# Kernel tuning notes

Measured on AMD Instinct MI355X. Metric: run time of the kernel, lower is better.

The kernel has to match this reference:

```python
import jax, jax.numpy as jnp
import numpy as np

N_NODES, N_EDGES, NUM_GRAPHS = 50000, 800000, 64
F_DIM, H_DIM, N_LAYERS, N_CLASSES = 64, 64, 3, 16
EPS = 1e-5  # StdAggregation epsilon (PyG)


def setup_inputs() -> dict:
    key = jax.random.key(0)
    ks = jax.random.split(key, 12)
    s = 0.05
    x = jax.random.normal(ks[0], (N_NODES, F_DIM), jnp.float32)
    edge_index = jax.random.randint(ks[1], (2, N_EDGES), 0, N_NODES, dtype=jnp.int32)
    batch = jnp.sort(jax.random.randint(ks[2], (N_NODES,), 0, NUM_GRAPHS, dtype=jnp.int32))
    # per-layer PNAConv params (towers=1): pre Linear(2F->F), post Linear(13F->H), lin Linear(H->H)
    pre_w = jax.random.normal(ks[3], (N_LAYERS, F_DIM, 2 * F_DIM), jnp.float32) * s
    pre_b = jnp.zeros((N_LAYERS, F_DIM), jnp.float32)
    post_w = jax.random.normal(ks[4], (N_LAYERS, H_DIM, 13 * F_DIM), jnp.float32) * s
    post_b = jnp.zeros((N_LAYERS, H_DIM), jnp.float32)
    lin_w = jax.random.normal(ks[5], (N_LAYERS, H_DIM, H_DIM), jnp.float32) * s
    lin_b = jnp.zeros((N_LAYERS, H_DIM), jnp.float32)
    mlp_w1 = jax.random.normal(ks[6], (H_DIM, H_DIM), jnp.float32) * s
    mlp_b1 = jnp.zeros((H_DIM,), jnp.float32)
    mlp_w2 = jax.random.normal(ks[7], (N_CLASSES, H_DIM), jnp.float32) * s
    mlp_b2 = jnp.zeros((N_CLASSES,), jnp.float32)
    return dict(x=x, edge_index=edge_index, batch=batch,
                pre_w=pre_w, pre_b=pre_b, post_w=post_w, post_b=post_b,
                lin_w=lin_w, lin_b=lin_b, mlp_w1=mlp_w1, mlp_b1=mlp_b1,
                mlp_w2=mlp_w2, mlp_b2=mlp_b2)


def pna_forward(x, src, dst, pre_w, pre_b, post_w, post_b, lin_w, lin_b,
                mlp_w1, mlp_b1, mlp_w2, mlp_b2, batch):
    N = x.shape[0]
    deg_raw = jax.ops.segment_sum(jnp.ones_like(src, jnp.float32), dst, N)  # in-degree [N]
    deg = jnp.maximum(deg_raw, 1.0)[:, None]
    # avg log degree (PNA avg_deg['log'] from the degree histogram of this graph)
    avg_log = jnp.mean(jnp.log(deg_raw + 1.0))
    log_deg = jnp.log(deg + 1.0)
    amp = log_deg / avg_log          # amplification scaler [N,1]
    att = avg_log / log_deg          # attenuation scaler [N,1]
    has_in = (deg_raw > 0)[:, None]

    for l in range(pre_w.shape[0]):
        h = jnp.concatenate([x[dst], x[src]], axis=-1)        # [E, 2F] (x_i, x_j)
        m = h @ pre_w[l].T + pre_b[l]                          # pre_nn message [E, F]
        s1 = jax.ops.segment_sum(m, dst, N)
        s2 = jax.ops.segment_sum(m * m, dst, N)
        mean = s1 / deg
        std = jnp.sqrt(jax.nn.relu(s2 / deg - mean * mean) + EPS)
        mn = jnp.where(has_in, jax.ops.segment_min(m, dst, N), 0.0)
        mx = jnp.where(has_in, jax.ops.segment_max(m, dst, N), 0.0)
        aggr = jnp.concatenate([mean, mn, mx, std], axis=-1)   # [N, 4F]
        out = jnp.concatenate([x, aggr, aggr * amp, aggr * att], axis=-1)  # [N, 13F]
        out = out @ post_w[l].T + post_b[l]                    # post_nn [N, H]
        x = jax.nn.relu(out @ lin_w[l].T + lin_b[l])           # conv.lin + outer ReLU

    # global mean pool over graphs
    counts = jnp.maximum(
        jax.ops.segment_sum(jnp.ones((N,), x.dtype), batch, NUM_GRAPHS), 1.0)
    g = jax.ops.segment_sum(x, batch, NUM_GRAPHS) / counts[:, None]  # [G, H]
    g = jax.nn.relu(g @ mlp_w1.T + mlp_b1)
    return g @ mlp_w2.T + mlp_b2                               # [G, C]


def reference(x, edge_index, batch, pre_w, pre_b, post_w, post_b,
              lin_w, lin_b, mlp_w1, mlp_b1, mlp_w2, mlp_b2):
    src, dst = edge_index[0], edge_index[1]
    return pna_forward(x, src, dst, pre_w, pre_b, post_w, post_b,
                       lin_w, lin_b, mlp_w1, mlp_b1, mlp_w2, mlp_b2, batch)
```

## Files before the change

### kernel.cpp

```cpp
#include <hip/hip_runtime.h>
#include <math.h>

#define N_NODES   50000
#define N_EDGES   800000
#define NUM_GRAPHS 64
#define FDIM      64
#define HDIM      64
#define NLAYERS   3
#define NCLASSES  16
#define EPS       1e-5f

#define SCAN_CHUNK 1024
#define NCHUNKS ((N_NODES + SCAN_CHUNK - 1) / SCAN_CHUNK)

typedef unsigned short u16;
typedef unsigned int   u32;
typedef __attribute__((ext_vector_type(8))) short short8;
typedef __attribute__((ext_vector_type(4))) float floatx4;

#define WKS_LAYER 159744
#define PRES_LAYER 24576

__device__ inline void split1(float f, u16& h, u16& m, u16& l) {
    u32 b  = __float_as_uint(f);
    u32 hb = b & 0xFFFF0000u;
    float r = f - __uint_as_float(hb);
    u32 mb = __float_as_uint(r) & 0xFFFF0000u;
    float r2 = r - __uint_as_float(mb);
    u32 lb = __float_as_uint(r2) & 0xFFFF0000u;
    h = (u16)(hb >> 16); m = (u16)(mb >> 16); l = (u16)(lb >> 16);
}

__device__ inline void gl_lds16(const void* g, void* l) {
    __builtin_amdgcn_global_load_lds(
        (const __attribute__((address_space(1))) u32*)g,
        (__attribute__((address_space(3))) u32*)l, 16, 0, 0);
}

__global__ __launch_bounds__(256) void k_comb(const float* __restrict__ post_w,
                                              const float* __restrict__ lin_w,
                                              const float* __restrict__ pre_w,
                                              const float* __restrict__ post_b,
                                              const float* __restrict__ lin_b,
                                              u16* __restrict__ WkS,
                                              u16* __restrict__ PreS,
                                              float* __restrict__ bcv,
                                              int* __restrict__ cnt,
                                              float* __restrict__ logsum) {
    int b = blockIdx.x, t = threadIdx.x;
    int zi = b * 256 + t;
    if (zi < N_NODES) cnt[zi] = 0;
    if (zi == 0) *logsum = 0.f;

    if (b < 624) {
        int c  = t & 63;
        int kl = t >> 6;
        int l  = b / 208;
        int o  = (b % 208) * 4 + kl;
        const float* lw = lin_w + (size_t)l * 4096 + c * 64;
        const float* pw = post_w + (size_t)l * 53248 + o;
        float acc = 0.f;
        #pragma unroll 8
        for (int j = 0; j < 64; ++j)
            acc += lw[j] * pw[(size_t)j * 832];
        u16 h, m, lo;
        split1(acc, h, m, lo);

        int kn;
        if (o < 64) kn = o;
        else {
            int s  = (o - 64) >> 8;
            int mm = (o - 64) & 255;
            int j  = mm >> 5, r = mm & 31;
            kn = 64 + j * 96 + s * 32 + r;
        }
        int ch  = kn >> 5;
        int kin = kn & 31;
        int n16 = c & 15, nt = c >> 4;
        int swk = (((kin >> 3) + (n16 >> 1)) & 3) * 8 + (kin & 7);
        size_t base = (size_t)l * WKS_LAYER + (size_t)ch * 6144
                    + nt * 512 + n16 * 32 + swk;
        WkS[base]        = h;
        WkS[base + 2048] = m;
        WkS[base + 4096] = lo;
    } else if (b == 624) {
        if (t < 192) {
            int l = t >> 6, c = t & 63;
            float acc = lin_b[l * 64 + c];
            for (int j = 0; j < 64; ++j)
                acc += lin_w[(size_t)l * 4096 + c * 64 + j] * post_b[l * 64 + j];
            bcv[l * 64 + c] = acc;
        }
    } else {
        int i = (b - 625) * 256 + t;
        int l = i >> 13;
        int rem = i & 8191;
        int c128 = rem >> 6;
        int k = rem & 63;
        float v;
        if (c128 < 64) v = pre_w[(size_t)l * 8192 + c128 * 128 + k];
        else           v = pre_w[(size_t)l * 8192 + (c128 - 64) * 128 + 64 + k];
        u16 h, m, lo;
        split1(v, h, m, lo);
        int ch = k >> 5, kin = k & 31;
        int nt = c128 >> 4, n16 = c128 & 15;
        int swk = (((kin >> 3) + (n16 >> 1)) & 3) * 8 + (kin & 7);
        size_t base = (size_t)l * PRES_LAYER + (size_t)ch * 12288
                    + nt * 512 + n16 * 32 + swk;
        PreS[base]        = h;
        PreS[base + 4096] = m;
        PreS[base + 8192] = lo;
    }
}

__global__ void k_count(const int* __restrict__ dst, int* __restrict__ cnt,
                        int* __restrict__ rank) {
    int e = blockIdx.x * 256 + threadIdx.x;
    if (e < N_EDGES) rank[e] = atomicAdd(&cnt[dst[e]], 1);
}

__global__ void k_chunk_sums(const int* __restrict__ cnt, int* __restrict__ bsum,
                             float* __restrict__ logsum) {
    __shared__ int   ired[256];
    __shared__ float lred[256];
    int b = blockIdx.x, t = threadIdx.x;
    int base = b * SCAN_CHUNK;
    int s = 0; float ls = 0.f;
    for (int i = t; i < SCAN_CHUNK; i += 256) {
        int idx = base + i;
        if (idx < N_NODES) {
            int v = cnt[idx];
            s += v;
            ls += logf((float)v + 1.0f);
        }
    }
    ired[t] = s; lred[t] = ls;
    __syncthreads();
    for (int off = 128; off > 0; off >>= 1) {
        if (t < off) { ired[t] += ired[t + off]; lred[t] += lred[t + off]; }
        __syncthreads();
    }
    if (t == 0) { bsum[b] = ired[0]; atomicAdd(logsum, lred[0]); }
}

__global__ void k_scan_top(const int* __restrict__ bsum, int* __restrict__ boff,
                           int* __restrict__ row_start) {
    if (threadIdx.x == 0) {
        int acc = 0;
        for (int i = 0; i < NCHUNKS; ++i) { boff[i] = acc; acc += bsum[i]; }
        row_start[N_NODES] = acc;
    }
}

__global__ void k_scan_chunks(const int* __restrict__ cnt, const int* __restrict__ boff,
                              int* __restrict__ row_start) {
    __shared__ int tsum[256];
    int b = blockIdx.x, t = threadIdx.x;
    int base = b * SCAN_CHUNK + t * 4;
    int v[4]; int s = 0;
    #pragma unroll
    for (int i = 0; i < 4; ++i) {
        int idx = base + i;
        v[i] = (idx < N_NODES) ? cnt[idx] : 0;
        s += v[i];
    }
    tsum[t] = s;
    __syncthreads();
    for (int off = 1; off < 256; off <<= 1) {
        int val = (t >= off) ? tsum[t - off] : 0;
        __syncthreads();
        tsum[t] += val;
        __syncthreads();
    }
    int excl = boff[b] + tsum[t] - s;
    #pragma unroll
    for (int i = 0; i < 4; ++i) {
        int idx = base + i;
        if (idx < N_NODES) row_start[idx] = excl;
        excl += v[i];
    }
}

__global__ void k_scatter(const int* __restrict__ src, const int* __restrict__ dst,
                          const int* __restrict__ rank,
                          const int* __restrict__ row_start,
                          int* __restrict__ csr_src) {
    int e = blockIdx.x * 256 + threadIdx.x;
    if (e < N_EDGES) {
        int d = dst[e];
        csr_src[row_start[d] + rank[e]] = src[e];
    }
}

__global__ void k_scal(const int* __restrict__ cnt, const float* __restrict__ logsum,
                       float* __restrict__ inv_deg, float* __restrict__ ampv,
                       float* __restrict__ attv, float* __restrict__ g_sum,
                       int* __restrict__ g_cnt) {
    int n = blockIdx.x * 256 + threadIdx.x;
    if (blockIdx.x == 0) {
        for (int i = threadIdx.x; i < 4096; i += 256) g_sum[i] = 0.f;
        if (threadIdx.x < 64) g_cnt[threadIdx.x] = 0;
    }
    if (n < N_NODES) {
        float avg = logsum[0] / (float)N_NODES;
        float degf = fmaxf((float)cnt[n], 1.0f);
        inv_deg[n] = 1.0f / degf;
        float ld = logf(degf + 1.0f);
        ampv[n] = ld / avg;
        attv[n] = avg / ld;
    }
}

__global__ __launch_bounds__(256, 4) void k_pre(const float* __restrict__ x,
                                                const u16* __restrict__ PreS,
                                                const float* __restrict__ pre_b,
                                                float* __restrict__ p,
                                                float* __restrict__ q) {
    __shared__ u16 ldsB[2 * 12288];
    int t = threadIdx.x;
    int w = t >> 6;
    int lane = t & 63;
    int m = lane & 15;
    int qh = lane >> 4;
    int rowBase = blockIdx.x * 64;

    int myrow = rowBase + 16 * w + m;
    bool vr = myrow < N_NODES;
    int crow = vr ? myrow : 0;
    const float* xrow = x + (size_t)crow * 64;

    int bo = m * 32 + ((qh + (m >> 1)) & 3) * 8;

    #pragma unroll
    for (int ch = 0; ch < 2; ++ch) {
        const char* g = (const char*)PreS + (size_t)ch * 24576 + w * 6144 + lane * 16;
        char* l = (char*)ldsB + ch * 24576 + w * 6144;
        #pragma unroll
        for (int i = 0; i < 6; ++i)
            gl_lds16(g + i * 1024, l + i * 1024);
    }
    float fa[2][8];
    #pragma unroll
    for (int ch = 0; ch < 2; ++ch) {
        const float* sp = xrow + ch * 32 + qh * 8;
        float4 u0 = *(const float4*)sp;
        float4 u1 = *(const float4*)(sp + 4);
        fa[ch][0] = vr ? u0.x : 0.f; fa[ch][1] = vr ? u0.y : 0.f;
        fa[ch][2] = vr ? u0.z : 0.f; fa[ch][3] = vr ? u0.w : 0.f;
        fa[ch][4] = vr ? u1.x : 0.f; fa[ch][5] = vr ? u1.y : 0.f;
        fa[ch][6] = vr ? u1.z : 0.f; fa[ch][7] = vr ? u1.w : 0.f;
    }
    asm volatile("s_waitcnt vmcnt(0)" ::: "memory");
    __syncthreads();

    floatx4 acc[8] = {};
    #pragma unroll
    for (int ch = 0; ch < 2; ++ch) {
        union { u32 u[4]; short8 s8; } AH, AM, AL;
        #pragma unroll
        for (int i = 0; i < 4; ++i) {
            float f0 = fa[ch][2 * i], f1 = fa[ch][2 * i + 1];
            u32 b0 = __float_as_uint(f0), b1 = __float_as_uint(f1);
            u32 h0 = b0 & 0xFFFF0000u,  h1 = b1 & 0xFFFF0000u;
            float r0 = f0 - __uint_as_float(h0);
            float r1 = f1 - __uint_as_float(h1);
            u32 m0 = __float_as_uint(r0) & 0xFFFF0000u;
            u32 m1 = __float_as_uint(r1) & 0xFFFF0000u;
            float s0 = r0 - __uint_as_float(m0);
            float s1 = r1 - __uint_as_float(m1);
            u32 l0 = __float_as_uint(s0) & 0xFFFF0000u;
            u32 l1 = __float_as_uint(s1) & 0xFFFF0000u;
            AH.u[i] = (h0 >> 16) | h1;
            AM.u[i] = (m0 >> 16) | m1;
            AL.u[i] = (l0 >> 16) | l1;
        }
        const u16* Bb = ldsB + ch * 12288;
        #pragma unroll
        for (int nt = 0; nt < 8; ++nt) {
            short8 bH = *(const short8*)(Bb + nt * 512 + bo);
            short8 bM = *(const short8*)(Bb + 4096 + nt * 512 + bo);
            short8 bL = *(const short8*)(Bb + 8192 + nt * 512 + bo);
            acc[nt] = __builtin_amdgcn_mfma_f32_16x16x32_bf16(AH.s8, bH, acc[nt], 0, 0, 0);
            acc[nt] = __builtin_amdgcn_mfma_f32_16x16x32_bf16(AH.s8, bM, acc[nt], 0, 0, 0);
            acc[nt] = __builtin_amdgcn_mfma_f32_16x16x32_bf16(AM.s8, bH, acc[nt], 0, 0, 0);
            acc[nt] = __builtin_amdgcn_mfma_f32_16x16x32_bf16(AH.s8, bL, acc[nt], 0, 0, 0);
            acc[nt] = __builtin_amdgcn_mfma_f32_16x16x32_bf16(AM.s8, bM, acc[nt], 0, 0, 0);
            acc[nt] = __builtin_amdgcn_mfma_f32_16x16x32_bf16(AL.s8, bH, acc[nt], 0, 0, 0);
        }
    }

    int col = m;
    #pragma unroll
    for (int nt = 0; nt < 8; ++nt) {
        int cbase = (nt & 3) * 16 + col;
        float bias = (nt < 4) ? pre_b[cbase] : 0.f;
        float* outp = (nt < 4) ? p : q;
        #pragma unroll
        for (int reg = 0; reg < 4; ++reg) {
            int grow = rowBase + 16 * w + qh * 4 + reg;
            if (grow < N_NODES)
                outp[(size_t)grow * 64 + cbase] = acc[nt][reg] + bias;
        }
    }
}

__global__ __launch_bounds__(256) void k_aggr(const float* __restrict__ p,
                                              const float* __restrict__ q,
                                              const int* __restrict__ row_start,
                                              const int* __restrict__ csr_src,
                                              const float* __restrict__ inv_deg,
                                              float* __restrict__ aggr) {
    int wid  = (blockIdx.x * 256 + threadIdx.x) >> 6;
    int lane = threadIdx.x & 63;
    if (wid >= N_NODES) return;
    int n = wid;
    int beg = row_start[n], end = row_start[n + 1];
    float sum = 0.f, sq = 0.f;
    float mn = INFINITY, mx = -INFINITY;
    int e = beg;
    for (; e + 7 < end; e += 8) {
        float qv[8];
        #pragma unroll
        for (int u = 0; u < 8; ++u) {
            int s = csr_src[e + u];
            qv[u] = q[(size_t)s * 64 + lane];
        }
        #pragma unroll
        for (int u = 0; u < 8; ++u) {
            float m = qv[u];
            sum += m; sq += m * m;
            mn = fminf(mn, m); mx = fmaxf(mx, m);
        }
    }
    for (; e + 3 < end; e += 4) {
        float qv[4];
        #pragma unroll
        for (int u = 0; u < 4; ++u) {
            int s = csr_src[e + u];
            qv[u] = q[(size_t)s * 64 + lane];
        }
        #pragma unroll
        for (int u = 0; u < 4; ++u) {
            float m = qv[u];
            sum += m; sq += m * m;
            mn = fminf(mn, m); mx = fmaxf(mx, m);
        }
    }
    for (; e < end; ++e) {
        int s = csr_src[e];
        float m = q[(size_t)s * 64 + lane];
        sum += m; sq += m * m;
        mn = fminf(mn, m); mx = fmaxf(mx, m);
    }
    float* a = aggr + (size_t)n * 256;
    if (end <= beg) {
        a[lane]       = 0.f;
        a[64 + lane]  = 0.f;
        a[128 + lane] = 0.f;
        a[192 + lane] = sqrtf(EPS);
    } else {
        float pv = p[n * 64 + lane];
        float id = inv_deg[n];
        float meanq = sum * id;
        float var = fmaxf(sq * id - meanq * meanq, 0.f);
        a[lane]       = pv + meanq;
        a[64 + lane]  = pv + mn;
        a[128 + lane] = pv + mx;
        a[192 + lane] = sqrtf(var + EPS);
    }
}

#define DOMFMA(ACC0, ACC1)                                                     \
    {                                                                          \
        _Pragma("unroll")                                                      \
        for (int nt = 0; nt < 4; ++nt) {                                       \
            short8 bH = *(const short8*)(Bb + nt * 512 + bo);                  \
            short8 bM = *(const short8*)(Bb + 2048 + nt * 512 + bo);           \
            short8 bL = *(const short8*)(Bb + 4096 + nt * 512 + bo);           \
            ACC0[nt] = __builtin_amdgcn_mfma_f32_16x16x32_bf16(AH0.s8, bH, ACC0[nt], 0, 0, 0); \
            ACC0[nt] = __builtin_amdgcn_mfma_f32_16x16x32_bf16(AH0.s8, bM, ACC0[nt], 0, 0, 0); \
            ACC0[nt] = __builtin_amdgcn_mfma_f32_16x16x32_bf16(AM0.s8, bH, ACC0[nt], 0, 0, 0); \
            ACC0[nt] = __builtin_amdgcn_mfma_f32_16x16x32_bf16(AH0.s8, bL, ACC0[nt], 0, 0, 0); \
            ACC0[nt] = __builtin_amdgcn_mfma_f32_16x16x32_bf16(AM0.s8, bM, ACC0[nt], 0, 0, 0); \
            ACC0[nt] = __builtin_amdgcn_mfma_f32_16x16x32_bf16(AL0.s8, bH, ACC0[nt], 0, 0, 0); \
            ACC1[nt] = __builtin_amdgcn_mfma_f32_16x16x32_bf16(AH1.s8, bH, ACC1[nt], 0, 0, 0); \
            ACC1[nt] = __builtin_amdgcn_mfma_f32_16x16x32_bf16(AH1.s8, bM, ACC1[nt], 0, 0, 0); \
            ACC1[nt] = __builtin_amdgcn_mfma_f32_16x16x32_bf16(AM1.s8, bH, ACC1[nt], 0, 0, 0); \
            ACC1[nt] = __builtin_amdgcn_mfma_f32_16x16x32_bf16(AH1.s8, bL, ACC1[nt], 0, 0, 0); \
            ACC1[nt] = __builtin_amdgcn_mfma_f32_16x16x32_bf16(AM1.s8, bM, ACC1[nt], 0, 0, 0); \
            ACC1[nt] = __builtin_amdgcn_mfma_f32_16x16x32_bf16(AL1.s8, bH, ACC1[nt], 0, 0, 0); \
        }                                                                      \
    }

__global__ __launch_bounds__(256, 2) void k_post(const float* __restrict__ x,
                                                 const float* __restrict__ aggr,
                                                 const float* __restrict__ ampv,
                                                 const float* __restrict__ attv,
                                                 const u16* __restrict__ WkS,
                                                 const float* __restrict__ bc,
                                                 float* __restrict__ xout) {
    __shared__ u16 ldsB[3 * 6144];
    int t = threadIdx.x;
    int w = t >> 6;
    int lane = t & 63;
    int m = lane & 15;
    int qh = lane >> 4;
    int rowBase = blockIdx.x * 128;

    int row0 = rowBase + 32 * w + m;
    int row1 = row0 + 16;
    int cr0 = (row0 < N_NODES) ? row0 : 0;
    int cr1 = (row1 < N_NODES) ? row1 : 0;
    const float* xr0 = x + (size_t)cr0 * 64;
    const float* xr1 = x + (size_t)cr1 * 64;
    const float* ar0 = aggr + (size_t)cr0 * 256;
    const float* ar1 = aggr + (size_t)cr1 * 256;

    int bo = m * 32 + ((qh + (m >> 1)) & 3) * 8;

    floatx4 accP0[4] = {}, accA0[4] = {}, accT0[4] = {};
    floatx4 accP1[4] = {}, accA1[4] = {}, accT1[4] = {};

    float f0[8], f1[8];
    union U8 { u32 u[4]; short8 s8; };
    U8 AH0, AM0, AL0, AH1, AM1, AL1;

    auto gptr = [&](int g, const float* xr, const float* ar) -> const float* {
        return (g < 2) ? (xr + 32 * g) : (ar + (g - 2) * 32);
    };
    auto loadRaw = [&](const float* sp, float* f) {
        float4 u0 = *(const float4*)(sp + qh * 8);
        float4 u1 = *(const float4*)(sp + qh * 8 + 4);
        f[0] = u0.x; f[1] = u0.y; f[2] = u0.z; f[3] = u0.w;
        f[4] = u1.x; f[5] = u1.y; f[6] = u1.z; f[7] = u1.w;
    };
    auto stageIssue = [&](int ch, int buf) {
        const char* g = (const char*)WkS + (size_t)ch * 12288 + w * 3072 + lane * 16;
        char* l = (char*)ldsB + buf * 12288 + w * 3072;
        #pragma unroll
        for (int i = 0; i < 3; ++i)
            gl_lds16(g + i * 1024, l + i * 1024);
    };
    auto split2 = [&](const float* f, U8& H, U8& M8, U8& L) {
        #pragma unroll
        for (int i = 0; i < 4; ++i) {
            float v0 = f[2 * i], v1 = f[2 * i + 1];
            u32 b0 = __float_as_uint(v0), b1 = __float_as_uint(v1);
            u32 h0 = b0 & 0xFFFF0000u,  h1 = b1 & 0xFFFF0000u;
            float r0 = v0 - __uint_as_float(h0);
            float r1 = v1 - __uint_as_float(h1);
            u32 m0 = __float_as_uint(r0) & 0xFFFF0000u;
            u32 m1 = __float_as_uint(r1) & 0xFFFF0000u;
            float s0 = r0 - __uint_as_float(m0);
            float s1 = r1 - __uint_as_float(m1);
            u32 l0 = __float_as_uint(s0) & 0xFFFF0000u;
            u32 l1 = __float_as_uint(s1) & 0xFFFF0000u;
            H.u[i]  = (h0 >> 16) | h1;
            M8.u[i] = (m0 >> 16) | m1;
            L.u[i]  = (l0 >> 16) | l1;
        }
    };

    loadRaw(gptr(0, xr0, ar0), f0);
    loadRaw(gptr(0, xr1, ar1), f1);
    stageIssue(0, 0);
    stageIssue(1, 1);
    asm volatile("s_waitcnt vmcnt(3)" ::: "memory");
    asm volatile("s_barrier" ::: "memory");

    for (int ch = 0; ch < 26; ++ch) {
        int s = (ch < 2) ? 0 : (ch - 2) % 3;
        if (s == 0) {
            split2(f0, AH0, AM0, AL0);
            split2(f1, AH1, AM1, AL1);
        }
        bool pf = (ch + 1 < 26) && ((ch + 1 < 2) || ((ch + 1 - 2) % 3 == 0));
        if (pf) {
            int gn = (ch + 1 < 2) ? (ch + 1) : (2 + (ch + 1 - 2) / 3);
            loadRaw(gptr(gn, xr0, ar0), f0);
            loadRaw(gptr(gn, xr1, ar1), f1);
        }
        int ch2 = (ch + 2 < 26) ? ch + 2 : ch + 2 - 26;
        stageIssue(ch2, (ch + 2) % 3);

        const u16* Bb = ldsB + (ch % 3) * 6144;
        if (s == 0)      { DOMFMA(accP0, accP1); }
        else if (s == 1) { DOMFMA(accA0, accA1); }
        else             { DOMFMA(accT0, accT1); }

        if (pf) asm volatile("s_waitcnt vmcnt(7)" ::: "memory");
        else    asm volatile("s_waitcnt vmcnt(3)" ::: "memory");
        asm volatile("s_barrier" ::: "memory");
    }

    int col = m;
    #pragma unroll
    for (int frag = 0; frag < 2; ++frag) {
        #pragma unroll
        for (int reg = 0; reg < 4; ++reg) {
            int grow = rowBase + 32 * w + 16 * frag + qh * 4 + reg;
            if (grow < N_NODES) {
                float av = ampv[grow], tv = attv[grow];
                #pragma unroll
                for (int nt = 0; nt < 4; ++nt) {
                    float pv = frag ? accP1[nt][reg] : accP0[nt][reg];
                    float av2 = frag ? accA1[nt][reg] : accA0[nt][reg];
                    float tv2 = frag ? accT1[nt][reg] : accT0[nt][reg];
                    float v = pv + av * av2 + tv * tv2 + bc[nt * 16 + col];
                    xout[(size_t)grow * 64 + nt * 16 + col] = fmaxf(v, 0.f);
                }
            }
        }
    }
}
#undef DOMFMA

__global__ __launch_bounds__(256) void k_pool(const float* __restrict__ x,
                                              const int* __restrict__ batch,
                                              float* __restrict__ g_sum,
                                              int* __restrict__ g_cnt) {
    int lane = threadIdx.x & 63;
    int wave = blockIdx.x * 4 + (threadIdx.x >> 6);
    const int NPW = 16;
    int beg = wave * NPW;
    if (beg >= N_NODES) return;
    int end = min(beg + NPW, N_NODES);
    float acc = 0.f;
    int cur = batch[beg];
    int c = 0;
    for (int n = beg; n < end; ++n) {
        int b = batch[n];
        if (b != cur) {
            atomicAdd(&g_sum[cur * 64 + lane], acc);
            if (lane == 0) atomicAdd(&g_cnt[cur], c);
            acc = 0.f; c = 0; cur = b;
        }
        acc += x[n * 64 + lane];
        ++c;
    }
    atomicAdd(&g_sum[cur * 64 + lane], acc);
    if (lane == 0) atomicAdd(&g_cnt[cur], c);
}

__global__ __launch_bounds__(256) void k_mlp(const float* __restrict__ g_sum,
                                             const int* __restrict__ g_cnt,
                                             const float* __restrict__ w1,
                                             const float* __restrict__ b1,
                                             const float* __restrict__ w2,
                                             const float* __restrict__ b2,
                                             float* __restrict__ out) {
    __shared__ float g[64][64];
    __shared__ float h[64][64];
    __shared__ float wT[64][65];
    int t = threadIdx.x;
    for (int idx = t; idx < 4096; idx += 256) {
        int gi = idx >> 6, c = idx & 63;
        float cntf = fmaxf((float)g_cnt[gi], 1.f);
        g[gi][c] = g_sum[idx] / cntf;
    }
    for (int idx = t; idx < 4096; idx += 256) {
        int c = idx >> 6, k = idx & 63;
        wT[k][c] = w1[c * 64 + k];
    }
    __syncthreads();
    for (int idx = t; idx < 4096; idx += 256) {
        int gi = idx >> 6, c = idx & 63;
        float acc = b1[c];
        for (int k = 0; k < 64; ++k) acc += g[gi][k] * wT[k][c];
        h[gi][c] = fmaxf(acc, 0.f);
    }
    __syncthreads();
    for (int idx = t; idx < 64 * NCLASSES; idx += 256) {
        int gi = idx >> 4, c = idx & 15;
        float acc = b2[c];
        for (int k = 0; k < 64; ++k) acc += h[gi][k] * w2[c * 64 + k];
        out[gi * NCLASSES + c] = acc;
    }
}

extern "C" void kernel_launch(void* const* d_in, const int* in_sizes, int n_in,
                              void* d_out, int out_size, void* d_ws, size_t ws_size,
                              hipStream_t stream) {
    const float* x      = (const float*)d_in[0];
    const int*   ei     = (const int*)d_in[1];
    const int*   batch  = (const int*)d_in[2];
    const float* pre_w  = (const float*)d_in[3];
    const float* pre_b  = (const float*)d_in[4];
    const float* post_w = (const float*)d_in[5];
    const float* post_b = (const float*)d_in[6];
    const float* lin_w  = (const float*)d_in[7];
    const float* lin_b  = (const float*)d_in[8];
    const float* mlp_w1 = (const float*)d_in[9];
    const float* mlp_b1 = (const float*)d_in[10];
    const float* mlp_w2 = (const float*)d_in[11];
    const float* mlp_b2 = (const float*)d_in[12];

    const int* src = ei;
    const int* dst = ei + N_EDGES;

    char* base = (char*)d_ws;
    size_t off = 0;
    auto alloc = [&](size_t bytes) -> void* {
        void* ptr = base + off;
        off += (bytes + 255) & ~(size_t)255;
        return ptr;
    };
    int*   cnt       = (int*)alloc(N_NODES * 4);
    int*   row_start = (int*)alloc((N_NODES + 1) * 4);
    int*   rank      = (int*)alloc(N_EDGES * 4);
    int*   csr_src   = (int*)alloc(N_EDGES * 4);
    int*   bsum      = (int*)alloc(64 * 4);
    int*   boff      = (int*)alloc(64 * 4);
    float* logsum    = (float*)alloc(16);
    float* inv_deg   = (float*)alloc(N_NODES * 4);
    float* ampv      = (float*)alloc(N_NODES * 4);
    float* attv      = (float*)alloc(N_NODES * 4);
    float* p         = (float*)alloc((size_t)N_NODES * 64 * 4);
    float* q         = (float*)alloc((size_t)N_NODES * 64 * 4);
    float* aggr      = (float*)alloc((size_t)N_NODES * 256 * 4);
    float* xb0       = (float*)alloc((size_t)N_NODES * 64 * 4);
    float* xb1       = (float*)alloc((size_t)N_NODES * 64 * 4);
    float* g_sum     = (float*)alloc(64 * 64 * 4);
    int*   g_cnt     = (int*)alloc(64 * 4);
    u16*   WkS       = (u16*)alloc((size_t)3 * WKS_LAYER * 2);
    u16*   PreS      = (u16*)alloc((size_t)3 * PRES_LAYER * 2);
    float* bcv       = (float*)alloc(3 * 64 * 4);

    k_comb<<<721, 256, 0, stream>>>(post_w, lin_w, pre_w, post_b, lin_b,
                                    WkS, PreS, bcv, cnt, logsum);

    k_count<<<(N_EDGES + 255) / 256, 256, 0, stream>>>(dst, cnt, rank);
    k_chunk_sums<<<NCHUNKS, 256, 0, stream>>>(cnt, bsum, logsum);
    k_scan_top<<<1, 64, 0, stream>>>(bsum, boff, row_start);
    k_scan_chunks<<<NCHUNKS, 256, 0, stream>>>(cnt, boff, row_start);
    k_scatter<<<(N_EDGES + 255) / 256, 256, 0, stream>>>(src, dst, rank,
                                                         row_start, csr_src);
    k_scal<<<(N_NODES + 255) / 256, 256, 0, stream>>>(cnt, logsum, inv_deg,
                                                      ampv, attv, g_sum, g_cnt);

    const int PRE_BLOCKS  = (N_NODES + 63) / 64;
    const int POST_BLOCKS = (N_NODES + 127) / 128;
    const float* xin = x;
    float* bufs[3] = {xb0, xb1, xb0};
    for (int l = 0; l < NLAYERS; ++l) {
        k_pre<<<PRE_BLOCKS, 256, 0, stream>>>(xin, PreS + (size_t)l * PRES_LAYER,
                                              pre_b + l * 64, p, q);
        k_aggr<<<(N_NODES + 3) / 4, 256, 0, stream>>>(p, q, row_start, csr_src,
                                                      inv_deg, aggr);
        float* xo = bufs[l];
        k_post<<<POST_BLOCKS, 256, 0, stream>>>(xin, aggr, ampv, attv,
                                                WkS + (size_t)l * WKS_LAYER,
                                                bcv + l * 64, xo);
        xin = xo;
    }

    int pool_waves = (N_NODES + 15) / 16;
    k_pool<<<(pool_waves + 3) / 4, 256, 0, stream>>>(xin, batch, g_sum, g_cnt);
    k_mlp<<<1, 256, 0, stream>>>(g_sum, g_cnt, mlp_w1, mlp_b1, mlp_w2, mlp_b2,
                                 (float*)d_out);
}
```

Before: 482.3 us.

## Read post weights directly from global memory in single-wave k_post blocks

k_post drops its triple-buffered LDS staging of the split bf16 weight chunks, along with the async global-to-LDS copies and per-chunk barriers. Each 64-thread single-wave block now handles 32 rows and loads its B fragments straight from global/L2 into registers before issuing the MFMAs. This removes barrier and LDS overhead and allows many more independent blocks. In exchange, every wave refetches the full weight set from cache with no cross-wave reuse, and the weight loads are no longer pipelined ahead of the compute.

Result: slower. 492.9 us (+2.2%).

```diff
diff --git a/kernel.cpp b/kernel.cpp
--- a/kernel.cpp
+++ b/kernel.cpp
@@ -370,44 +370,19 @@
     }
 }
 
-#define DOMFMA(ACC0, ACC1)                                                     \
-    {                                                                          \
-        _Pragma("unroll")                                                      \
-        for (int nt = 0; nt < 4; ++nt) {                                       \
-            short8 bH = *(const short8*)(Bb + nt * 512 + bo);                  \
-            short8 bM = *(const short8*)(Bb + 2048 + nt * 512 + bo);           \
-            short8 bL = *(const short8*)(Bb + 4096 + nt * 512 + bo);           \
-            ACC0[nt] = __builtin_amdgcn_mfma_f32_16x16x32_bf16(AH0.s8, bH, ACC0[nt], 0, 0, 0); \
-            ACC0[nt] = __builtin_amdgcn_mfma_f32_16x16x32_bf16(AH0.s8, bM, ACC0[nt], 0, 0, 0); \
-            ACC0[nt] = __builtin_amdgcn_mfma_f32_16x16x32_bf16(AM0.s8, bH, ACC0[nt], 0, 0, 0); \
-            ACC0[nt] = __builtin_amdgcn_mfma_f32_16x16x32_bf16(AH0.s8, bL, ACC0[nt], 0, 0, 0); \
-            ACC0[nt] = __builtin_amdgcn_mfma_f32_16x16x32_bf16(AM0.s8, bM, ACC0[nt], 0, 0, 0); \
-            ACC0[nt] = __builtin_amdgcn_mfma_f32_16x16x32_bf16(AL0.s8, bH, ACC0[nt], 0, 0, 0); \
-            ACC1[nt] = __builtin_amdgcn_mfma_f32_16x16x32_bf16(AH1.s8, bH, ACC1[nt], 0, 0, 0); \
-            ACC1[nt] = __builtin_amdgcn_mfma_f32_16x16x32_bf16(AH1.s8, bM, ACC1[nt], 0, 0, 0); \
-            ACC1[nt] = __builtin_amdgcn_mfma_f32_16x16x32_bf16(AM1.s8, bH, ACC1[nt], 0, 0, 0); \
-            ACC1[nt] = __builtin_amdgcn_mfma_f32_16x16x32_bf16(AH1.s8, bL, ACC1[nt], 0, 0, 0); \
-            ACC1[nt] = __builtin_amdgcn_mfma_f32_16x16x32_bf16(AM1.s8, bM, ACC1[nt], 0, 0, 0); \
-            ACC1[nt] = __builtin_amdgcn_mfma_f32_16x16x32_bf16(AL1.s8, bH, ACC1[nt], 0, 0, 0); \
-        }                                                                      \
-    }
-
-__global__ __launch_bounds__(256, 2) void k_post(const float* __restrict__ x,
-                                                 const float* __restrict__ aggr,
-                                                 const float* __restrict__ ampv,
-                                                 const float* __restrict__ attv,
-                                                 const u16* __restrict__ WkS,
-                                                 const float* __restrict__ bc,
-                                                 float* __restrict__ xout) {
-    __shared__ u16 ldsB[3 * 6144];
-    int t = threadIdx.x;
-    int w = t >> 6;
-    int lane = t & 63;
+__global__ __launch_bounds__(64) void k_post(const float* __restrict__ x,
+                                             const float* __restrict__ aggr,
+                                             const float* __restrict__ ampv,
+                                             const float* __restrict__ attv,
+                                             const u16* __restrict__ WkS,
+                                             const float* __restrict__ bc,
+                                             float* __restrict__ xout) {
+    int lane = threadIdx.x;
     int m = lane & 15;
     int qh = lane >> 4;
-    int rowBase = blockIdx.x * 128;
-
-    int row0 = rowBase + 32 * w + m;
+    int rowBase = blockIdx.x * 32;
+
+    int row0 = rowBase + m;
     int row1 = row0 + 16;
     int cr0 = (row0 < N_NODES) ? row0 : 0;
     int cr1 = (row1 < N_NODES) ? row1 : 0;
@@ -417,6 +392,7 @@
     const float* ar1 = aggr + (size_t)cr1 * 256;
 
     int bo = m * 32 + ((qh + (m >> 1)) & 3) * 8;
+    const u16* Wb = WkS + bo;
 
     floatx4 accP0[4] = {}, accA0[4] = {}, accT0[4] = {};
     floatx4 accP1[4] = {}, accA1[4] = {}, accT1[4] = {};
@@ -425,21 +401,11 @@
     union U8 { u32 u[4]; short8 s8; };
     U8 AH0, AM0, AL0, AH1, AM1, AL1;
 
-    auto gptr = [&](int g, const float* xr, const float* ar) -> const float* {
-        return (g < 2) ? (xr + 32 * g) : (ar + (g - 2) * 32);
-    };
     auto loadRaw = [&](const float* sp, float* f) {
         float4 u0 = *(const float4*)(sp + qh * 8);
         float4 u1 = *(const float4*)(sp + qh * 8 + 4);
         f[0] = u0.x; f[1] = u0.y; f[2] = u0.z; f[3] = u0.w;
         f[4] = u1.x; f[5] = u1.y; f[6] = u1.z; f[7] = u1.w;
-    };
-    auto stageIssue = [&](int ch, int buf) {
-        const char* g = (const char*)WkS + (size_t)ch * 12288 + w * 3072 + lane * 16;
-        char* l = (char*)ldsB + buf * 12288 + w * 3072;
-        #pragma unroll
-        for (int i = 0; i < 3; ++i)
-            gl_lds16(g + i * 1024, l + i * 1024);
     };
     auto split2 = [&](const float* f, U8& H, U8& M8, U8& L) {
         #pragma unroll
@@ -460,37 +426,46 @@
             L.u[i]  = (l0 >> 16) | l1;
         }
     };
-
-    loadRaw(gptr(0, xr0, ar0), f0);
-    loadRaw(gptr(0, xr1, ar1), f1);
-    stageIssue(0, 0);
-    stageIssue(1, 1);
-    asm volatile("s_waitcnt vmcnt(3)" ::: "memory");
-    asm volatile("s_barrier" ::: "memory");
-
-    for (int ch = 0; ch < 26; ++ch) {
-        int s = (ch < 2) ? 0 : (ch - 2) % 3;
-        if (s == 0) {
-            split2(f0, AH0, AM0, AL0);
-            split2(f1, AH1, AM1, AL1);
-        }
-        bool pf = (ch + 1 < 26) && ((ch + 1 < 2) || ((ch + 1 - 2) % 3 == 0));
-        if (pf) {
-            int gn = (ch + 1 < 2) ? (ch + 1) : (2 + (ch + 1 - 2) / 3);
-            loadRaw(gptr(gn, xr0, ar0), f0);
-            loadRaw(gptr(gn, xr1, ar1), f1);
-        }
-        int ch2 = (ch + 2 < 26) ? ch + 2 : ch + 2 - 26;
-        stageIssue(ch2, (ch + 2) % 3);
-
-        const u16* Bb = ldsB + (ch % 3) * 6144;
-        if (s == 0)      { DOMFMA(accP0, accP1); }
-        else if (s == 1) { DOMFMA(accA0, accA1); }
-        else             { DOMFMA(accT0, accT1); }
-
-        if (pf) asm volatile("s_waitcnt vmcnt(7)" ::: "memory");
-        else    asm volatile("s_waitcnt vmcnt(3)" ::: "memory");
-        asm volatile("s_barrier" ::: "memory");
+    auto chunkMM = [&](int ch, floatx4* A0, floatx4* A1) {
+        const u16* pB = Wb + ch * 6144;
+        short8 bH[4], bM[4], bL[4];
+        #pragma unroll
+        for (int nt = 0; nt < 4; ++nt) {
+            bH[nt] = *(const short8*)(pB + nt * 512);
+            bM[nt] = *(const short8*)(pB + 2048 + nt * 512);
+            bL[nt] = *(const short8*)(pB + 4096 + nt * 512);
+        }
+        #pragma unroll
+        for (int nt = 0; nt < 4; ++nt) {
+            A0[nt] = __builtin_amdgcn_mfma_f32_16x16x32_bf16(AH0.s8, bH[nt], A0[nt], 0, 0, 0);
+            A0[nt] = __builtin_amdgcn_mfma_f32_16x16x32_bf16(AH0.s8, bM[nt], A0[nt], 0, 0, 0);
+            A0[nt] = __builtin_amdgcn_mfma_f32_16x16x32_bf16(AM0.s8, bH[nt], A0[nt], 0, 0, 0);
+            A0[nt] = __builtin_amdgcn_mfma_f32_16x16x32_bf16(AH0.s8, bL[nt], A0[nt], 0, 0, 0);
+            A0[nt] = __builtin_amdgcn_mfma_f32_16x16x32_bf16(AM0.s8, bM[nt], A0[nt], 0, 0, 0);
+            A0[nt] = __builtin_amdgcn_mfma_f32_16x16x32_bf16(AL0.s8, bH[nt], A0[nt], 0, 0, 0);
+            A1[nt] = __builtin_amdgcn_mfma_f32_16x16x32_bf16(AH1.s8, bH[nt], A1[nt], 0, 0, 0);
+            A1[nt] = __builtin_amdgcn_mfma_f32_16x16x32_bf16(AH1.s8, bM[nt], A1[nt], 0, 0, 0);
+            A1[nt] = __builtin_amdgcn_mfma_f32_16x16x32_bf16(AM1.s8, bH[nt], A1[nt], 0, 0, 0);
+            A1[nt] = __builtin_amdgcn_mfma_f32_16x16x32_bf16(AH1.s8, bL[nt], A1[nt], 0, 0, 0);
+            A1[nt] = __builtin_amdgcn_mfma_f32_16x16x32_bf16(AM1.s8, bM[nt], A1[nt], 0, 0, 0);
+            A1[nt] = __builtin_amdgcn_mfma_f32_16x16x32_bf16(AL1.s8, bH[nt], A1[nt], 0, 0, 0);
+        }
+    };
+
+    loadRaw(xr0, f0); loadRaw(xr1, f1);
+    split2(f0, AH0, AM0, AL0); split2(f1, AH1, AM1, AL1);
+    loadRaw(xr0 + 32, f0); loadRaw(xr1 + 32, f1);
+    chunkMM(0, accP0, accP1);
+    split2(f0, AH0, AM0, AL0); split2(f1, AH1, AM1, AL1);
+    loadRaw(ar0, f0); loadRaw(ar1, f1);
+    chunkMM(1, accP0, accP1);
+    for (int j = 0; j < 8; ++j) {
+        split2(f0, AH0, AM0, AL0); split2(f1, AH1, AM1, AL1);
+        if (j < 7) { loadRaw(ar0 + (j + 1) * 32, f0); loadRaw(ar1 + (j + 1) * 32, f1); }
+        int ch = 2 + 3 * j;
+        chunkMM(ch,     accP0, accP1);
+        chunkMM(ch + 1, accA0, accA1);
+        chunkMM(ch + 2, accT0, accT1);
     }
 
     int col = m;
@@ -498,12 +473,12 @@
     for (int frag = 0; frag < 2; ++frag) {
         #pragma unroll
         for (int reg = 0; reg < 4; ++reg) {
-            int grow = rowBase + 32 * w + 16 * frag + qh * 4 + reg;
+            int grow = rowBase + 16 * frag + qh * 4 + reg;
             if (grow < N_NODES) {
                 float av = ampv[grow], tv = attv[grow];
                 #pragma unroll
                 for (int nt = 0; nt < 4; ++nt) {
-                    float pv = frag ? accP1[nt][reg] : accP0[nt][reg];
+                    float pv  = frag ? accP1[nt][reg] : accP0[nt][reg];
                     float av2 = frag ? accA1[nt][reg] : accA0[nt][reg];
                     float tv2 = frag ? accT1[nt][reg] : accT0[nt][reg];
                     float v = pv + av * av2 + tv * tv2 + bc[nt * 16 + col];
@@ -513,7 +488,6 @@
         }
     }
 }
-#undef DOMFMA
 
 __global__ __launch_bounds__(256) void k_pool(const float* __restrict__ x,
                                               const int* __restrict__ batch,
@@ -639,7 +613,7 @@
                                                       ampv, attv, g_sum, g_cnt);
 
     const int PRE_BLOCKS  = (N_NODES + 63) / 64;
-    const int POST_BLOCKS = (N_NODES + 127) / 128;
+    const int POST_BLOCKS = (N_NODES + 31) / 32;
     const float* xin = x;
     float* bufs[3] = {xb0, xb1, xb0};
     for (int l = 0; l < NLAYERS; ++l) {
@@ -648,9 +622,9 @@
         k_aggr<<<(N_NODES + 3) / 4, 256, 0, stream>>>(p, q, row_start, csr_src,
                                                       inv_deg, aggr);
         float* xo = bufs[l];
-        k_post<<<POST_BLOCKS, 256, 0, stream>>>(xin, aggr, ampv, attv,
-                                                WkS + (size_t)l * WKS_LAYER,
-                                                bcv + l * 64, xo);
+        k_post<<<POST_BLOCKS, 64, 0, stream>>>(xin, aggr, ampv, attv,
+                                               WkS + (size_t)l * WKS_LAYER,
+                                               bcv + l * 64, xo);
         xin = xo;
     }
 
```
